# Kernel optimization log

Hardware: AMD Instinct MI355X
Metric: run time of the kernel (lower is better)

## Reference

```python
import jax, jax.numpy as jnp
import numpy as np
from jax import lax


def _median_blur(img, k):
    # img: [B, H, W]; k odd (3 here). Replicate border like cv2.medianBlur.
    p = k // 2
    B, H, W = img.shape
    xp = jnp.pad(img, ((0, 0), (p, p), (p, p)), mode='edge')
    # Gather the k*k shifted views -> [B, H, W, k*k]
    wins = jnp.stack([xp[:, i:i + H, j:j + W] for i in range(k) for j in range(k)], axis=-1)
    return jnp.median(wins, axis=-1)


def setup_inputs() -> dict:
    key = jax.random.key(0)
    kx, kt = jax.random.split(key)
    x = jax.random.normal(kx, (32, 1, 512, 512), dtype=jnp.float32)
    t_tensor = jax.random.randint(kt, (32,), 0, 10).astype(jnp.int64)
    return {"x": x, "t_tensor": t_tensor, "kernel_size": 3, "num_timesteps": 10}


def reference(x, t_tensor, kernel_size, num_timesteps):
    # Faithful vectorized version of MedianBlur.forward_process:
    # sample i gets t_tensor[i] successive median blurs.
    B, C, H, W = x.shape  # C == 1, matching the .squeeze() in the original
    img = x[:, 0, :, :]  # [B, H, W]
    t = t_tensor.astype(jnp.int32)

    def step(cur, j):
        blurred = _median_blur(cur, kernel_size)
        active = (j < t)[:, None, None]  # only samples with t_i > j keep blurring
        return jnp.where(active, blurred, cur), None

    out, _ = lax.scan(step, img, jnp.arange(num_timesteps, dtype=jnp.int32))
    return out[:, None, :, :]  # restore channel dim, like unsqueeze(0) per sample
```

## Files before the change

kernel.cpp:

```cpp
#include <hip/hip_runtime.h>


#define TD 82
#define OW 64
#define RAD 9
#define NT 256

__device__ __forceinline__ float min3f(float a, float b, float c) { return fminf(fminf(a, b), c); }
__device__ __forceinline__ float max3f(float a, float b, float c) { return fmaxf(fmaxf(a, b), c); }
__device__ __forceinline__ float med3f(float a, float b, float c) { return __builtin_amdgcn_fmed3f(a, b, c); }

__global__ __launch_bounds__(NT, 6) void median_fused_kernel(
    const float* __restrict__ src, float* __restrict__ dst,
    const int* __restrict__ t)
{
    __shared__ float buf[TD * TD];

    const int b   = blockIdx.y;
    const int y0  = (blockIdx.x >> 3) * OW;
    const int x0  = (blockIdx.x & 7) * OW;
    const int tid = threadIdx.x;
    const float* img  = src + (b << 18);
    float*       outb = dst + (b << 18);

    int T = t[b];
    T = min(max(T, 0), 9);

    const int sr = tid >> 4;
    const int sc = (tid & 15) << 2;

    if (T == 0) {
        #pragma unroll
        for (int rr = 0; rr < 4; ++rr) {
            int gy = y0 + sr + rr * 16;
            *(float4*)&outb[(gy << 9) + x0 + sc] =
                *(const float4*)&img[(gy << 9) + x0 + sc];
        }
        return;
    }

    for (int i = tid; i < TD * TD; i += NT) {
        int r = i / TD, c = i - r * TD;
        int gy = min(max(y0 - RAD + r, 0), 511);
        int gx = min(max(x0 - RAD + c, 0), 511);
        buf[i] = img[(gy << 9) + gx];
    }

    const bool topE = (y0 == 0),   botE = (y0 == 512 - OW);
    const bool lftE = (x0 == 0),   rgtE = (x0 == 512 - OW);

    const int ptx = tid & 15;
    const int pty = tid >> 4;
    const int ub  = 1 + 5 * pty;
    const int vb  = 1 + 5 * ptx;
    float* wrow = &buf[ub * TD + vb];

    const bool padTop = topE && (pty == 1);
    const bool padBot = botE && (pty == 14);
    const bool padLft = lftE && (ptx == 1);
    const bool padRgt = rgtE && (ptx == 14);

    __syncthreads();

    for (int k = 0; k < T; ++k) {
        float A[7], Br[7], C[7], stage[25];
        const float* p = &buf[(ub - 1) * TD + (vb - 1)];
        #pragma unroll
        for (int j = 0; j < 7; ++j) A[j] = p[j];
        p += TD;
        #pragma unroll
        for (int j = 0; j < 7; ++j) Br[j] = p[j];
        #pragma unroll
        for (int i = 0; i < 5; ++i) {
            p += TD;
            #pragma unroll
            for (int j = 0; j < 7; ++j) C[j] = p[j];
            float lo[7], mi[7], hi[7];
            #pragma unroll
            for (int j = 0; j < 7; ++j) {
                lo[j] = min3f(A[j], Br[j], C[j]);
                mi[j] = med3f(A[j], Br[j], C[j]);
                hi[j] = max3f(A[j], Br[j], C[j]);
            }
            #pragma unroll
            for (int j = 0; j < 5; ++j)
                stage[i * 5 + j] = med3f(max3f(lo[j], lo[j+1], lo[j+2]),
                                         med3f(mi[j], mi[j+1], mi[j+2]),
                                         min3f(hi[j], hi[j+1], hi[j+2]));
            #pragma unroll
            for (int j = 0; j < 7; ++j) { A[j] = Br[j]; Br[j] = C[j]; }
        }
        __syncthreads();
        #pragma unroll
        for (int i = 0; i < 5; ++i)
            #pragma unroll
            for (int j = 0; j < 5; ++j)
                wrow[i * TD + j] = stage[i * 5 + j];
        if (padTop) {
            #pragma unroll
            for (int j = 0; j < 5; ++j) buf[8 * TD + vb + j] = stage[15 + j];
            if (padLft) buf[8 * TD + 8]  = stage[18];
            if (padRgt) buf[8 * TD + 73] = stage[16];
        }
        if (padBot) {
            #pragma unroll
            for (int j = 0; j < 5; ++j) buf[73 * TD + vb + j] = stage[5 + j];
            if (padLft) buf[73 * TD + 8]  = stage[8];
            if (padRgt) buf[73 * TD + 73] = stage[6];
        }
        if (padLft) {
            #pragma unroll
            for (int i = 0; i < 5; ++i) buf[(ub + i) * TD + 8] = stage[i * 5 + 3];
        }
        if (padRgt) {
            #pragma unroll
            for (int i = 0; i < 5; ++i) buf[(ub + i) * TD + 73] = stage[i * 5 + 1];
        }
        __syncthreads();
    }

    #pragma unroll
    for (int rr = 0; rr < 4; ++rr) {
        int row = sr + rr * 16;
        const float* s = &buf[(row + RAD) * TD + RAD + sc];
        float4 v = { s[0], s[1], s[2], s[3] };
        *(float4*)&outb[((y0 + row) << 9) + x0 + sc] = v;
    }
}

extern "C" void kernel_launch(void* const* d_in, const int* in_sizes, int n_in,
                              void* d_out, int out_size, void* d_ws, size_t ws_size,
                              hipStream_t stream) {
    const float* x   = (const float*)d_in[0];
    const int*   t   = (const int*)d_in[1];
    float*       out = (float*)d_out;

    dim3 block(NT);
    dim3 grid(64, 32);
    median_fused_kernel<<<grid, block, 0, stream>>>(x, out, t);
}
```

Baseline: 107.9 us.

## Keep each thread's 5x5 tile in registers, write only halo ring to LDS

```diff
diff --git a/kernel.cpp b/kernel.cpp
--- a/kernel.cpp
+++ b/kernel.cpp
@@ -10,7 +10,7 @@
 __device__ __forceinline__ float max3f(float a, float b, float c) { return fmaxf(fmaxf(a, b), c); }
 __device__ __forceinline__ float med3f(float a, float b, float c) { return __builtin_amdgcn_fmed3f(a, b, c); }
 
-__global__ __launch_bounds__(NT, 6) void median_fused_kernel(
+__global__ __launch_bounds__(NT) void median_fused_kernel(
     const float* __restrict__ src, float* __restrict__ dst,
     const int* __restrict__ t)
 {
@@ -46,14 +46,13 @@
         buf[i] = img[(gy << 9) + gx];
     }
 
-    const bool topE = (y0 == 0),   botE = (y0 == 512 - OW);
-    const bool lftE = (x0 == 0),   rgtE = (x0 == 512 - OW);
+    const bool topE = (y0 == 0), botE = (y0 == 512 - OW);
+    const bool lftE = (x0 == 0), rgtE = (x0 == 512 - OW);
 
     const int ptx = tid & 15;
     const int pty = tid >> 4;
     const int ub  = 1 + 5 * pty;
     const int vb  = 1 + 5 * ptx;
-    float* wrow = &buf[ub * TD + vb];
 
     const bool padTop = topE && (pty == 1);
     const bool padBot = botE && (pty == 14);
@@ -62,19 +61,37 @@
 
     __syncthreads();
 
+    float stage[25];
+    #pragma unroll
+    for (int i = 0; i < 5; ++i)
+        #pragma unroll
+        for (int j = 0; j < 5; ++j)
+            stage[i * 5 + j] = buf[(ub + i) * TD + vb + j];
+
     for (int k = 0; k < T; ++k) {
-        float A[7], Br[7], C[7], stage[25];
-        const float* p = &buf[(ub - 1) * TD + (vb - 1)];
+        float A[7], Br[7], C[7], ns[25];
+        {
+            const float* p = &buf[(ub - 1) * TD + (vb - 1)];
+            #pragma unroll
+            for (int j = 0; j < 7; ++j) A[j] = p[j];
+        }
+        Br[0] = buf[ub * TD + (vb - 1)];
         #pragma unroll
-        for (int j = 0; j < 7; ++j) A[j] = p[j];
-        p += TD;
-        #pragma unroll
-        for (int j = 0; j < 7; ++j) Br[j] = p[j];
+        for (int j = 0; j < 5; ++j) Br[1 + j] = stage[j];
+        Br[6] = buf[ub * TD + (vb + 5)];
+
         #pragma unroll
         for (int i = 0; i < 5; ++i) {
-            p += TD;
-            #pragma unroll
-            for (int j = 0; j < 7; ++j) C[j] = p[j];
+            if (i < 4) {
+                C[0] = buf[(ub + 1 + i) * TD + (vb - 1)];
+                #pragma unroll
+                for (int j = 0; j < 5; ++j) C[1 + j] = stage[(i + 1) * 5 + j];
+                C[6] = buf[(ub + 1 + i) * TD + (vb + 5)];
+            } else {
+                const float* p = &buf[(ub + 5) * TD + (vb - 1)];
+                #pragma unroll
+                for (int j = 0; j < 7; ++j) C[j] = p[j];
+            }
             float lo[7], mi[7], hi[7];
             #pragma unroll
             for (int j = 0; j < 7; ++j) {
@@ -84,38 +101,53 @@
             }
             #pragma unroll
             for (int j = 0; j < 5; ++j)
-                stage[i * 5 + j] = med3f(max3f(lo[j], lo[j+1], lo[j+2]),
-                                         med3f(mi[j], mi[j+1], mi[j+2]),
-                                         min3f(hi[j], hi[j+1], hi[j+2]));
+                ns[i * 5 + j] = med3f(max3f(lo[j], lo[j+1], lo[j+2]),
+                                      med3f(mi[j], mi[j+1], mi[j+2]),
+                                      min3f(hi[j], hi[j+1], hi[j+2]));
             #pragma unroll
             for (int j = 0; j < 7; ++j) { A[j] = Br[j]; Br[j] = C[j]; }
         }
-        __syncthreads();
-        #pragma unroll
-        for (int i = 0; i < 5; ++i)
-            #pragma unroll
-            for (int j = 0; j < 5; ++j)
-                wrow[i * TD + j] = stage[i * 5 + j];
+
         if (padTop) {
             #pragma unroll
-            for (int j = 0; j < 5; ++j) buf[8 * TD + vb + j] = stage[15 + j];
-            if (padLft) buf[8 * TD + 8]  = stage[18];
-            if (padRgt) buf[8 * TD + 73] = stage[16];
+            for (int j = 0; j < 5; ++j) ns[10 + j] = ns[15 + j];
         }
         if (padBot) {
             #pragma unroll
-            for (int j = 0; j < 5; ++j) buf[73 * TD + vb + j] = stage[5 + j];
-            if (padLft) buf[73 * TD + 8]  = stage[8];
-            if (padRgt) buf[73 * TD + 73] = stage[6];
+            for (int j = 0; j < 5; ++j) ns[10 + j] = ns[5 + j];
         }
         if (padLft) {
             #pragma unroll
-            for (int i = 0; i < 5; ++i) buf[(ub + i) * TD + 8] = stage[i * 5 + 3];
+            for (int i = 0; i < 5; ++i) ns[i * 5 + 2] = ns[i * 5 + 3];
         }
         if (padRgt) {
             #pragma unroll
-            for (int i = 0; i < 5; ++i) buf[(ub + i) * TD + 73] = stage[i * 5 + 1];
+            for (int i = 0; i < 5; ++i) ns[i * 5 + 2] = ns[i * 5 + 1];
         }
+
+        __syncthreads();
+
+        if (k == T - 1) {
+            #pragma unroll
+            for (int i = 0; i < 5; ++i)
+                #pragma unroll
+                for (int j = 0; j < 5; ++j)
+                    buf[(ub + i) * TD + vb + j] = ns[i * 5 + j];
+        } else {
+            #pragma unroll
+            for (int j = 0; j < 5; ++j) buf[ub * TD + vb + j]       = ns[j];
+            #pragma unroll
+            for (int j = 0; j < 5; ++j) buf[(ub + 4) * TD + vb + j] = ns[20 + j];
+            #pragma unroll
+            for (int i = 1; i < 4; ++i) {
+                buf[(ub + i) * TD + vb]     = ns[i * 5];
+                buf[(ub + i) * TD + vb + 4] = ns[i * 5 + 4];
+            }
+        }
+
+        #pragma unroll
+        for (int m = 0; m < 25; ++m) stage[m] = ns[m];
+
         __syncthreads();
     }
 
```

New measurement: 104.5 us. 3.2% less time.
